# Kernel optimization log

Measured on AMD Instinct MI355X. Metric: run time of the kernel, lower is better.

## Reference

```python
import jax, jax.numpy as jnp
import numpy as np

N, M, D = 1024, 32, 512


def setup_inputs() -> dict:
    key = jax.random.key(0)
    k1, = jax.random.split(key, 1)
    emb = jax.random.normal(k1, (N, M, D), dtype=jnp.float32)
    emb = emb / jnp.linalg.norm(emb, axis=-1, keepdims=True)  # module expects normed embeddings
    return {
        "normed_embedding": emb,
        "n": N,
        "m": M,
        "ln_w": jnp.array(10.0, dtype=jnp.float32),
        "ln_b": jnp.array(-5.0, dtype=jnp.float32),
    }


def reference(normed_embedding, n, m, ln_w, ln_b):
    # normed_embedding: [N, M, D]
    ck = jnp.mean(normed_embedding, axis=1)          # [N, D] inclusive centroids
    sums = jnp.sum(normed_embedding, axis=1)         # [N, D]
    e = normed_embedding.reshape(n * m, -1)          # [NM, D]
    sims = jnp.matmul(e, ck.T)                       # [NM, N]

    # exclusive centroid for own speaker: cj = (sum_i - e_ij) / (m - 1)
    ex = jnp.sum(normed_embedding * (sums[:, None, :] - normed_embedding), axis=-1) / (m - 1)  # [N, M]
    rows = jnp.arange(n * m)
    spk = rows // m                                  # speaker label per row
    sims = sims.at[rows, spk].set(ex.reshape(-1))

    sims = jax.nn.sigmoid(ln_w * sims + ln_b)

    own = sims[rows, spk]                            # [NM]
    own_col = spk[:, None] == jnp.arange(n)[None, :]  # mask own speaker column
    max_other = jnp.max(jnp.where(own_col, -jnp.inf, sims), axis=-1)  # [NM]
    loss = jnp.mean(1.0 - own + max_other).reshape(1)

    preds = jnp.argmax(sims, axis=1)
    batch_acc = jnp.mean((preds == spk).astype(jnp.float32))
    return loss, batch_acc
```

## Files before the change

### kernel.cpp

```cpp
#include <hip/hip_runtime.h>


#define N_SPK 1024
#define M_UTT 32
#define D_DIM 512
#define NROWS (N_SPK * M_UTT)
#define NTILES 8
#define MTILES 256
#define NWG (MTILES * NTILES)
#define NKT 8

typedef __attribute__((ext_vector_type(4))) float f32x4;

__device__ __forceinline__ void gload_lds16(const void* g, void* l) {
    __builtin_amdgcn_global_load_lds(
        (const __attribute__((address_space(1))) unsigned int*)g,
        (__attribute__((address_space(3))) unsigned int*)l, 16, 0, 0);
}

__device__ __forceinline__ float sigmoidf(float x) {
    return 1.f / (1.f + __expf(-x));
}

__global__ void __launch_bounds__(256) prep_kernel(const float* __restrict__ emb,
                                                   const float* __restrict__ lnw,
                                                   unsigned int* __restrict__ e8,
                                                   unsigned int* __restrict__ ck8) {
    __shared__ float part[2][D_DIM];
    const int n = blockIdx.x;
    const int t = threadIdx.x;
    const int d4 = (t & 127) * 4;
    const int mh = t >> 7;
    const float* base = emb + (size_t)n * M_UTT * D_DIM;

    float4 acc = {0.f, 0.f, 0.f, 0.f};
#pragma unroll
    for (int mm = 0; mm < 16; ++mm) {
        const int m = mh * 16 + mm;
        const float4 v = *reinterpret_cast<const float4*>(base + m * D_DIM + d4);
        acc.x += v.x; acc.y += v.y; acc.z += v.z; acc.w += v.w;
        int w = __builtin_amdgcn_cvt_pk_fp8_f32(8.f * v.x, 8.f * v.y, 0, false);
        w = __builtin_amdgcn_cvt_pk_fp8_f32(8.f * v.z, 8.f * v.w, w, true);
        e8[(((size_t)(n * M_UTT + m)) * D_DIM + d4) >> 2] = (unsigned int)w;
    }
    *reinterpret_cast<float4*>(&part[mh][d4]) = acc;
    __syncthreads();
    if (t < 128) {
        const float sgn = (lnw[0] >= 0.f) ? 1.f : -1.f;
        const float sc = sgn * 0.5f;
        const int d = t * 4;
        const float4 a = *reinterpret_cast<const float4*>(&part[0][d]);
        const float4 b = *reinterpret_cast<const float4*>(&part[1][d]);
        int w = __builtin_amdgcn_cvt_pk_fp8_f32((a.x + b.x) * sc, (a.y + b.y) * sc, 0, false);
        w = __builtin_amdgcn_cvt_pk_fp8_f32((a.z + b.z) * sc, (a.w + b.w) * sc, w, true);
        ck8[(((size_t)n) * D_DIM + d) >> 2] = (unsigned int)w;
    }
}

__global__ void __launch_bounds__(256, 3)
gemm_kernel(const char* __restrict__ e8,
            const char* __restrict__ ck8,
            float* __restrict__ maxo_part,
            float* __restrict__ own_part) {
    __shared__ __align__(16) char buf[2][16384];
    __shared__ float redm[2][128];
    __shared__ float redo[2][128];

    const int tid  = threadIdx.x;
    const int lane = tid & 63;
    const int wv   = tid >> 6;
    const int lo   = lane & 15;
    const int hi   = lane >> 4;
    const int wm   = wv >> 1;
    const int wn   = wv & 1;

    const int raw   = blockIdx.x;
    const int xcd   = raw & 7;
    const int local = raw >> 3;
    const int mt    = xcd * 32 + (local >> 3);
    const int nt    = local & 7;
    const int r0    = mt * 128;
    const int n0    = nt * 128;

    const char* pA[2];
    const char* pB[2];
    int dA[2], dB[2];
#pragma unroll
    for (int j = 0; j < 2; ++j) {
        const int s   = j * 256 + tid;
        const int L   = s >> 3;
        const int l   = (s & 7) ^ (L & 7);
        const int row = 2 * L + (l >> 2);
        const int kch = l & 3;
        pA[j] = e8  + (size_t)(r0 + row) * D_DIM + kch * 16;
        pB[j] = ck8 + (size_t)(n0 + row) * D_DIM + kch * 16;
        dA[j] = s * 16;
        dB[j] = 8192 + s * 16;
    }

    auto stage = [&](int u) {
        char* bb = &buf[u & 1][0];
        const int ko = u * 64;
#pragma unroll
        for (int j = 0; j < 2; ++j) {
            gload_lds16(pA[j] + ko, bb + dA[j]);
            gload_lds16(pB[j] + ko, bb + dB[j]);
        }
    };

    stage(0);
    asm volatile("s_waitcnt vmcnt(0)" ::: "memory");
    __builtin_amdgcn_s_barrier();

    const int Lr    = lo >> 1;
    const int par   = lo & 1;
    const int phys0 = ((par << 2) | (hi >> 1))     ^ Lr;
    const int phys1 = ((par << 2) | 2 | (hi >> 1)) ^ Lr;
    const int a0 = (wm * 32 + Lr) * 128 + phys0 * 16 + (hi & 1) * 8;
    const int a1 = (wm * 32 + Lr) * 128 + phys1 * 16 + (hi & 1) * 8;
    const int b0 = 8192 + (wn * 32 + Lr) * 128 + phys0 * 16 + (hi & 1) * 8;
    const int b1 = 8192 + (wn * 32 + Lr) * 128 + phys1 * 16 + (hi & 1) * 8;

    f32x4 acc[4][4];
#pragma unroll
    for (int am = 0; am < 4; ++am)
#pragma unroll
        for (int an = 0; an < 4; ++an) acc[am][an] = (f32x4){0.f, 0.f, 0.f, 0.f};

    long a[4], b[4];

#pragma unroll
    for (int t = 0; t < NKT; ++t) {
        const char* bp = &buf[t & 1][0];
        if (t < NKT - 1) stage(t + 1);

#pragma unroll
        for (int am = 0; am < 4; ++am)
            a[am] = *reinterpret_cast<const long*>(bp + a0 + am * 1024);
#pragma unroll
        for (int an = 0; an < 4; ++an)
            b[an] = *reinterpret_cast<const long*>(bp + b0 + an * 1024);
        __builtin_amdgcn_s_setprio(1);
#pragma unroll
        for (int am = 0; am < 4; ++am)
#pragma unroll
            for (int an = 0; an < 4; ++an)
                acc[am][an] = __builtin_amdgcn_mfma_f32_16x16x32_fp8_fp8(
                    a[am], b[an], acc[am][an], 0, 0, 0);
        __builtin_amdgcn_s_setprio(0);

#pragma unroll
        for (int am = 0; am < 4; ++am)
            a[am] = *reinterpret_cast<const long*>(bp + a1 + am * 1024);
#pragma unroll
        for (int an = 0; an < 4; ++an)
            b[an] = *reinterpret_cast<const long*>(bp + b1 + an * 1024);
        __builtin_amdgcn_s_setprio(1);
#pragma unroll
        for (int am = 0; am < 4; ++am)
#pragma unroll
            for (int an = 0; an < 4; ++an)
                acc[am][an] = __builtin_amdgcn_mfma_f32_16x16x32_fp8_fp8(
                    a[am], b[an], acc[am][an], 0, 0, 0);
        __builtin_amdgcn_s_setprio(0);

        asm volatile("s_waitcnt lgkmcnt(0)" ::: "memory");
        if (t < NKT - 1) asm volatile("s_waitcnt vmcnt(0)" ::: "memory");
        __builtin_amdgcn_s_barrier();
    }

    const float NEG = -1e30f;
#pragma unroll
    for (int am = 0; am < 4; ++am) {
#pragma unroll
        for (int reg = 0; reg < 4; ++reg) {
            const int rl   = wm * 64 + am * 16 + hi * 4 + reg;
            const int rowg = r0 + rl;
            const int spk  = rowg >> 5;
            float m = NEG, o = NEG;
#pragma unroll
            for (int an = 0; an < 4; ++an) {
                const int col = n0 + wn * 64 + an * 16 + lo;
                const float v = acc[am][an][reg];
                const bool dg = (col == spk);
                o = dg ? v : o;
                m = fmaxf(m, dg ? NEG : v);
            }
#pragma unroll
            for (int mask = 1; mask < 16; mask <<= 1) {
                m = fmaxf(m, __shfl_xor(m, mask));
                o = fmaxf(o, __shfl_xor(o, mask));
            }
            if (lo == 0) {
                redm[wn][rl] = m;
                redo[wn][rl] = o;
            }
        }
    }
    __syncthreads();

    if (tid < 128) {
        const float mo = fmaxf(redm[0][tid], redm[1][tid]);
        maxo_part[(size_t)nt * NROWS + r0 + tid] = mo;
        if (nt == (mt >> 5)) {
            own_part[r0 + tid] = fmaxf(redo[0][tid], redo[1][tid]);
        }
    }
}

__global__ void __launch_bounds__(256) rowred_kernel(const float* __restrict__ maxo_part,
                                                     const float* __restrict__ own_part,
                                                     const float* __restrict__ lnw,
                                                     const float* __restrict__ lnb,
                                                     float* __restrict__ partsum) {
    const int r = blockIdx.x * 256 + threadIdx.x;
    const float lw = lnw[0], lb = lnb[0];
    const float sgn = (lw >= 0.f) ? 1.f : -1.f;
    const float alw = fabsf(lw);
    const float inv128 = 1.f / 128.f;

    float mo = maxo_part[r];
#pragma unroll
    for (int p = 1; p < NTILES; ++p)
        mo = fmaxf(mo, maxo_part[(size_t)p * NROWS + r]);
    const float O     = own_part[r];
    const float t_own = sgn * O * inv128;
    const float ex    = (32.f * t_own - 1.f) * (1.f / 31.f);
    const float own_s = sigmoidf(lw * ex + lb);
    const float mo_s  = sigmoidf(alw * mo * inv128 + lb);
    float loss = 1.f - own_s + mo_s;
    float corr = (sgn * ex >= mo * inv128) ? 1.f : 0.f;

#pragma unroll
    for (int mask = 1; mask < 64; mask <<= 1) {
        loss += __shfl_xor(loss, mask);
        corr += __shfl_xor(corr, mask);
    }
    __shared__ float sl[4], sc[4];
    const int wv = threadIdx.x >> 6;
    if ((threadIdx.x & 63) == 0) { sl[wv] = loss; sc[wv] = corr; }
    __syncthreads();
    if (threadIdx.x == 0) {
        partsum[blockIdx.x]       = sl[0] + sl[1] + sl[2] + sl[3];
        partsum[128 + blockIdx.x] = sc[0] + sc[1] + sc[2] + sc[3];
    }
}

__global__ void __launch_bounds__(128) final_kernel(const float* __restrict__ partsum,
                                                    float* __restrict__ out) {
    const int t = threadIdx.x;
    float l = partsum[t];
    float c = partsum[128 + t];
#pragma unroll
    for (int mask = 1; mask < 64; mask <<= 1) {
        l += __shfl_xor(l, mask);
        c += __shfl_xor(c, mask);
    }
    __shared__ float sl[2], sc[2];
    if ((t & 63) == 0) { sl[t >> 6] = l; sc[t >> 6] = c; }
    __syncthreads();
    if (t == 0) {
        out[0] = (sl[0] + sl[1]) * (1.f / (float)NROWS);
        out[1] = (sc[0] + sc[1]) * (1.f / (float)NROWS);
    }
}

extern "C" void kernel_launch(void* const* d_in, const int* in_sizes, int n_in,
                              void* d_out, int out_size, void* d_ws, size_t ws_size,
                              hipStream_t stream) {
    (void)in_sizes; (void)n_in; (void)out_size; (void)ws_size;
    const float* emb = (const float*)d_in[0];
    const float* lnw = (const float*)d_in[3];
    const float* lnb = (const float*)d_in[4];
    float* out = (float*)d_out;

    char* ws = (char*)d_ws;
    char* e8  = ws;
    char* ck8 = ws + (size_t)NROWS * D_DIM;
    float* maxo_part = (float*)(ck8 + (size_t)N_SPK * D_DIM);
    float* own_part  = (float*)((char*)maxo_part + (size_t)NTILES * NROWS * 4);
    float* partsum   = (float*)((char*)own_part + (size_t)NROWS * 4);

    prep_kernel<<<N_SPK, 256, 0, stream>>>(emb, lnw, (unsigned int*)e8, (unsigned int*)ck8);
    gemm_kernel<<<NWG, 256, 0, stream>>>(e8, ck8, maxo_part, own_part);
    rowred_kernel<<<NROWS / 256, 256, 0, stream>>>(maxo_part, own_part, lnw, lnb, partsum);
    final_kernel<<<1, 128, 0, stream>>>(partsum, out);
}
```

Before: 56.88 us.

## Triple-buffer GEMM LDS staging and permute fp8 layout for 16-byte fragment loads

The prep kernel now writes fp8 embeddings and centroids in a permuted K order, so that each lane's two MFMA k-slices sit next to each other. The GEMM can then fetch both with a single 16-byte LDS read instead of two 8-byte reads. The GEMM also moves from double to triple buffering: it prefetches two K-tiles ahead and waits with vmcnt(4) instead of draining all loads each iteration, to hide global-load latency. The cost is 48KB of LDS per workgroup instead of 32KB, which may lower occupancy under the 3-blocks-per-CU launch bound. The new layout must match exactly between the prep and GEMM kernels.

```diff
diff --git a/kernel.cpp b/kernel.cpp
--- a/kernel.cpp
+++ b/kernel.cpp
@@ -11,6 +11,7 @@
 #define NKT 8
 
 typedef __attribute__((ext_vector_type(4))) float f32x4;
+typedef __attribute__((ext_vector_type(2))) long long2v;
 
 __device__ __forceinline__ void gload_lds16(const void* g, void* l) {
     __builtin_amdgcn_global_load_lds(
@@ -24,36 +25,52 @@
 
 __global__ void __launch_bounds__(256) prep_kernel(const float* __restrict__ emb,
                                                    const float* __restrict__ lnw,
-                                                   unsigned int* __restrict__ e8,
-                                                   unsigned int* __restrict__ ck8) {
-    __shared__ float part[2][D_DIM];
+                                                   char* __restrict__ e8,
+                                                   char* __restrict__ ck8) {
+    __shared__ float part[4][D_DIM];
     const int n = blockIdx.x;
     const int t = threadIdx.x;
-    const int d4 = (t & 127) * 4;
-    const int mh = t >> 7;
-    const float* base = emb + (size_t)n * M_UTT * D_DIM;
-
-    float4 acc = {0.f, 0.f, 0.f, 0.f};
-#pragma unroll
-    for (int mm = 0; mm < 16; ++mm) {
-        const int m = mh * 16 + mm;
-        const float4 v = *reinterpret_cast<const float4*>(base + m * D_DIM + d4);
-        acc.x += v.x; acc.y += v.y; acc.z += v.z; acc.w += v.w;
-        int w = __builtin_amdgcn_cvt_pk_fp8_f32(8.f * v.x, 8.f * v.y, 0, false);
-        w = __builtin_amdgcn_cvt_pk_fp8_f32(8.f * v.z, 8.f * v.w, w, true);
-        e8[(((size_t)(n * M_UTT + m)) * D_DIM + d4) >> 2] = (unsigned int)w;
-    }
-    *reinterpret_cast<float4*>(&part[mh][d4]) = acc;
-    __syncthreads();
-    if (t < 128) {
-        const float sgn = (lnw[0] >= 0.f) ? 1.f : -1.f;
-        const float sc = sgn * 0.5f;
-        const int d = t * 4;
-        const float4 a = *reinterpret_cast<const float4*>(&part[0][d]);
-        const float4 b = *reinterpret_cast<const float4*>(&part[1][d]);
-        int w = __builtin_amdgcn_cvt_pk_fp8_f32((a.x + b.x) * sc, (a.y + b.y) * sc, 0, false);
-        w = __builtin_amdgcn_cvt_pk_fp8_f32((a.z + b.z) * sc, (a.w + b.w) * sc, w, true);
-        ck8[(((size_t)n) * D_DIM + d) >> 2] = (unsigned int)w;
+    const int q = t & 63;
+    const int g = t >> 6;
+    const int pdst = (q >> 3) * 64 + (q & 3) * 16 + ((q >> 2) & 1) * 8;
+    const float* base = emb + (size_t)n * M_UTT * D_DIM + q * 8;
+
+    float acc8[8];
+#pragma unroll
+    for (int j = 0; j < 8; ++j) acc8[j] = 0.f;
+
+#pragma unroll
+    for (int i = 0; i < 8; ++i) {
+        const int m = g * 8 + i;
+        const float4 v0 = *reinterpret_cast<const float4*>(base + m * D_DIM);
+        const float4 v1 = *reinterpret_cast<const float4*>(base + m * D_DIM + 4);
+        acc8[0] += v0.x; acc8[1] += v0.y; acc8[2] += v0.z; acc8[3] += v0.w;
+        acc8[4] += v1.x; acc8[5] += v1.y; acc8[6] += v1.z; acc8[7] += v1.w;
+        int w0 = __builtin_amdgcn_cvt_pk_fp8_f32(8.f * v0.x, 8.f * v0.y, 0, false);
+        w0 = __builtin_amdgcn_cvt_pk_fp8_f32(8.f * v0.z, 8.f * v0.w, w0, true);
+        int w1 = __builtin_amdgcn_cvt_pk_fp8_f32(8.f * v1.x, 8.f * v1.y, 0, false);
+        w1 = __builtin_amdgcn_cvt_pk_fp8_f32(8.f * v1.z, 8.f * v1.w, w1, true);
+        uint2 w; w.x = (unsigned)w0; w.y = (unsigned)w1;
+        *reinterpret_cast<uint2*>(e8 + (size_t)(n * M_UTT + m) * D_DIM + pdst) = w;
+    }
+#pragma unroll
+    for (int j = 0; j < 8; ++j) part[g][q * 8 + j] = acc8[j];
+    __syncthreads();
+
+    if (t < 64) {
+        const float sc = (lnw[0] >= 0.f) ? 0.5f : -0.5f;
+        float s[8];
+#pragma unroll
+        for (int j = 0; j < 8; ++j)
+            s[j] = (part[0][t * 8 + j] + part[1][t * 8 + j] +
+                    part[2][t * 8 + j] + part[3][t * 8 + j]) * sc;
+        int w0 = __builtin_amdgcn_cvt_pk_fp8_f32(s[0], s[1], 0, false);
+        w0 = __builtin_amdgcn_cvt_pk_fp8_f32(s[2], s[3], w0, true);
+        int w1 = __builtin_amdgcn_cvt_pk_fp8_f32(s[4], s[5], 0, false);
+        w1 = __builtin_amdgcn_cvt_pk_fp8_f32(s[6], s[7], w1, true);
+        uint2 w; w.x = (unsigned)w0; w.y = (unsigned)w1;
+        const int pd = (t >> 3) * 64 + (t & 3) * 16 + ((t >> 2) & 1) * 8;
+        *reinterpret_cast<uint2*>(ck8 + (size_t)n * D_DIM + pd) = w;
     }
 }
 
@@ -62,7 +79,7 @@
             const char* __restrict__ ck8,
             float* __restrict__ maxo_part,
             float* __restrict__ own_part) {
-    __shared__ __align__(16) char buf[2][16384];
+    __shared__ __align__(16) char buf[3][16384];
     __shared__ float redm[2][128];
     __shared__ float redo[2][128];
 
@@ -91,15 +108,15 @@
         const int L   = s >> 3;
         const int l   = (s & 7) ^ (L & 7);
         const int row = 2 * L + (l >> 2);
-        const int kch = l & 3;
-        pA[j] = e8  + (size_t)(r0 + row) * D_DIM + kch * 16;
-        pB[j] = ck8 + (size_t)(n0 + row) * D_DIM + kch * 16;
+        const int c   = l & 3;
+        pA[j] = e8  + (size_t)(r0 + row) * D_DIM + c * 16;
+        pB[j] = ck8 + (size_t)(n0 + row) * D_DIM + c * 16;
         dA[j] = s * 16;
         dB[j] = 8192 + s * 16;
     }
 
-    auto stage = [&](int u) {
-        char* bb = &buf[u & 1][0];
+    auto stage = [&](int u, int slot) {
+        char* bb = &buf[slot][0];
         const int ko = u * 64;
 #pragma unroll
         for (int j = 0; j < 2; ++j) {
@@ -108,18 +125,16 @@
         }
     };
 
-    stage(0);
-    asm volatile("s_waitcnt vmcnt(0)" ::: "memory");
+    stage(0, 0);
+    stage(1, 1);
+    asm volatile("s_waitcnt vmcnt(4)" ::: "memory");
     __builtin_amdgcn_s_barrier();
 
-    const int Lr    = lo >> 1;
+    const int swz   = (lo >> 1) & 7;
     const int par   = lo & 1;
-    const int phys0 = ((par << 2) | (hi >> 1))     ^ Lr;
-    const int phys1 = ((par << 2) | 2 | (hi >> 1)) ^ Lr;
-    const int a0 = (wm * 32 + Lr) * 128 + phys0 * 16 + (hi & 1) * 8;
-    const int a1 = (wm * 32 + Lr) * 128 + phys1 * 16 + (hi & 1) * 8;
-    const int b0 = 8192 + (wn * 32 + Lr) * 128 + phys0 * 16 + (hi & 1) * 8;
-    const int b1 = 8192 + (wn * 32 + Lr) * 128 + phys1 * 16 + (hi & 1) * 8;
+    const int physr = ((par << 2) | hi) ^ swz;
+    const int abase = (wm * 32 + (lo >> 1)) * 128 + physr * 16;
+    const int bbase = 8192 + (wn * 32 + (lo >> 1)) * 128 + physr * 16;
 
     f32x4 acc[4][4];
 #pragma unroll
@@ -127,45 +142,37 @@
 #pragma unroll
         for (int an = 0; an < 4; ++an) acc[am][an] = (f32x4){0.f, 0.f, 0.f, 0.f};
 
-    long a[4], b[4];
-
 #pragma unroll
     for (int t = 0; t < NKT; ++t) {
-        const char* bp = &buf[t & 1][0];
-        if (t < NKT - 1) stage(t + 1);
-
+        const char* bp = &buf[t % 3][0];
+        if (t + 2 < NKT) stage(t + 2, (t + 2) % 3);
+
+        long2v a2[4], b2[4];
 #pragma unroll
         for (int am = 0; am < 4; ++am)
-            a[am] = *reinterpret_cast<const long*>(bp + a0 + am * 1024);
+            a2[am] = *reinterpret_cast<const long2v*>(bp + abase + am * 1024);
 #pragma unroll
         for (int an = 0; an < 4; ++an)
-            b[an] = *reinterpret_cast<const long*>(bp + b0 + an * 1024);
+            b2[an] = *reinterpret_cast<const long2v*>(bp + bbase + an * 1024);
+
         __builtin_amdgcn_s_setprio(1);
 #pragma unroll
         for (int am = 0; am < 4; ++am)
 #pragma unroll
             for (int an = 0; an < 4; ++an)
                 acc[am][an] = __builtin_amdgcn_mfma_f32_16x16x32_fp8_fp8(
-                    a[am], b[an], acc[am][an], 0, 0, 0);
-        __builtin_amdgcn_s_setprio(0);
-
-#pragma unroll
-        for (int am = 0; am < 4; ++am)
-            a[am] = *reinterpret_cast<const long*>(bp + a1 + am * 1024);
-#pragma unroll
-        for (int an = 0; an < 4; ++an)
-            b[an] = *reinterpret_cast<const long*>(bp + b1 + an * 1024);
-        __builtin_amdgcn_s_setprio(1);
+                    a2[am][0], b2[an][0], acc[am][an], 0, 0, 0);
 #pragma unroll
         for (int am = 0; am < 4; ++am)
 #pragma unroll
             for (int an = 0; an < 4; ++an)
                 acc[am][an] = __builtin_amdgcn_mfma_f32_16x16x32_fp8_fp8(
-                    a[am], b[an], acc[am][an], 0, 0, 0);
+                    a2[am][1], b2[an][1], acc[am][an], 0, 0, 0);
         __builtin_amdgcn_s_setprio(0);
 
         asm volatile("s_waitcnt lgkmcnt(0)" ::: "memory");
-        if (t < NKT - 1) asm volatile("s_waitcnt vmcnt(0)" ::: "memory");
+        if (t < NKT - 2)       asm volatile("s_waitcnt vmcnt(4)" ::: "memory");
+        else if (t == NKT - 2) asm volatile("s_waitcnt vmcnt(0)" ::: "memory");
         __builtin_amdgcn_s_barrier();
     }
 
@@ -281,7 +288,7 @@
     float* own_part  = (float*)((char*)maxo_part + (size_t)NTILES * NROWS * 4);
     float* partsum   = (float*)((char*)own_part + (size_t)NROWS * 4);
 
-    prep_kernel<<<N_SPK, 256, 0, stream>>>(emb, lnw, (unsigned int*)e8, (unsigned int*)ck8);
+    prep_kernel<<<N_SPK, 256, 0, stream>>>(emb, lnw, e8, ck8);
     gemm_kernel<<<NWG, 256, 0, stream>>>(e8, ck8, maxo_part, own_part);
     rowred_kernel<<<NROWS / 256, 256, 0, stream>>>(maxo_part, own_part, lnw, lnb, partsum);
     final_kernel<<<1, 128, 0, stream>>>(partsum, out);
```

After: 64.71 us. +13.8%, slower.

## Switch GEMM to 32x32x64 scaled FP8 MFMA with triple-buffered LDS pipeline

Applied to the files above, without the earlier changes.

Replaces the 16x16x32 FP8 MFMAs with the gfx950 scaled 32x32x64 f8f6f4 MFMA using unit scales, so each wave issues 4 large MFMAs per K-tile instead of 32 small ones and reads 16-byte LDS fragments. LDS staging goes from double to triple buffering, prefetching two tiles ahead with partial vmcnt waits. The epilogue row/column mapping and the shuffle reduction width are adapted to the 32x32 output layout. This drops the occupancy hint of 3 and raises LDS use, which may reduce occupancy.

```diff
diff --git a/kernel.cpp b/kernel.cpp
--- a/kernel.cpp
+++ b/kernel.cpp
@@ -10,7 +10,9 @@
 #define NWG (MTILES * NTILES)
 #define NKT 8
 
-typedef __attribute__((ext_vector_type(4))) float f32x4;
+typedef __attribute__((ext_vector_type(16))) float f32x16;
+typedef __attribute__((ext_vector_type(8)))  int   i32x8;
+typedef __attribute__((ext_vector_type(4)))  int   i32x4;
 
 __device__ __forceinline__ void gload_lds16(const void* g, void* l) {
     __builtin_amdgcn_global_load_lds(
@@ -57,20 +59,20 @@
     }
 }
 
-__global__ void __launch_bounds__(256, 3)
+__global__ void __launch_bounds__(256)
 gemm_kernel(const char* __restrict__ e8,
             const char* __restrict__ ck8,
             float* __restrict__ maxo_part,
             float* __restrict__ own_part) {
-    __shared__ __align__(16) char buf[2][16384];
+    __shared__ __align__(16) char buf[3][16384];
     __shared__ float redm[2][128];
     __shared__ float redo[2][128];
 
     const int tid  = threadIdx.x;
     const int lane = tid & 63;
     const int wv   = tid >> 6;
-    const int lo   = lane & 15;
-    const int hi   = lane >> 4;
+    const int l31  = lane & 31;
+    const int kg   = lane >> 5;
     const int wm   = wv >> 1;
     const int wn   = wv & 1;
 
@@ -91,15 +93,15 @@
         const int L   = s >> 3;
         const int l   = (s & 7) ^ (L & 7);
         const int row = 2 * L + (l >> 2);
-        const int kch = l & 3;
-        pA[j] = e8  + (size_t)(r0 + row) * D_DIM + kch * 16;
-        pB[j] = ck8 + (size_t)(n0 + row) * D_DIM + kch * 16;
+        const int c   = l & 3;
+        pA[j] = e8  + (size_t)(r0 + row) * D_DIM + c * 16;
+        pB[j] = ck8 + (size_t)(n0 + row) * D_DIM + c * 16;
         dA[j] = s * 16;
         dB[j] = 8192 + s * 16;
     }
 
-    auto stage = [&](int u) {
-        char* bb = &buf[u & 1][0];
+    auto stage = [&](int u, int slot) {
+        char* bb = &buf[slot][0];
         const int ko = u * 64;
 #pragma unroll
         for (int j = 0; j < 2; ++j) {
@@ -108,90 +110,97 @@
         }
     };
 
-    stage(0);
-    asm volatile("s_waitcnt vmcnt(0)" ::: "memory");
+    stage(0, 0);
+    stage(1, 1);
+    asm volatile("s_waitcnt vmcnt(4)" ::: "memory");
     __builtin_amdgcn_s_barrier();
 
-    const int Lr    = lo >> 1;
-    const int par   = lo & 1;
-    const int phys0 = ((par << 2) | (hi >> 1))     ^ Lr;
-    const int phys1 = ((par << 2) | 2 | (hi >> 1)) ^ Lr;
-    const int a0 = (wm * 32 + Lr) * 128 + phys0 * 16 + (hi & 1) * 8;
-    const int a1 = (wm * 32 + Lr) * 128 + phys1 * 16 + (hi & 1) * 8;
-    const int b0 = 8192 + (wn * 32 + Lr) * 128 + phys0 * 16 + (hi & 1) * 8;
-    const int b1 = 8192 + (wn * 32 + Lr) * 128 + phys1 * 16 + (hi & 1) * 8;
-
-    f32x4 acc[4][4];
-#pragma unroll
-    for (int am = 0; am < 4; ++am)
-#pragma unroll
-        for (int an = 0; an < 4; ++an) acc[am][an] = (f32x4){0.f, 0.f, 0.f, 0.f};
-
-    long a[4], b[4];
+    int aoff[2][2], boff[2][2];
+#pragma unroll
+    for (int am = 0; am < 2; ++am) {
+        const int r = wm * 64 + am * 32 + l31;
+        const int L = r >> 1, u = r & 1, s = L & 7;
+#pragma unroll
+        for (int h = 0; h < 2; ++h)
+            aoff[am][h] = L * 128 + ((((u << 2) | (kg * 2 + h)) ^ s) * 16);
+    }
+#pragma unroll
+    for (int an = 0; an < 2; ++an) {
+        const int r = wn * 64 + an * 32 + l31;
+        const int L = r >> 1, u = r & 1, s = L & 7;
+#pragma unroll
+        for (int h = 0; h < 2; ++h)
+            boff[an][h] = 8192 + L * 128 + ((((u << 2) | (kg * 2 + h)) ^ s) * 16);
+    }
+
+    f32x16 acc00 = {0.f}, acc01 = {0.f}, acc10 = {0.f}, acc11 = {0.f};
+#pragma unroll
+    for (int i = 0; i < 16; ++i) { acc00[i] = 0.f; acc01[i] = 0.f; acc10[i] = 0.f; acc11[i] = 0.f; }
+
+    const int SCALE1 = 0x7F7F7F7F;
 
 #pragma unroll
     for (int t = 0; t < NKT; ++t) {
-        const char* bp = &buf[t & 1][0];
-        if (t < NKT - 1) stage(t + 1);
-
-#pragma unroll
-        for (int am = 0; am < 4; ++am)
-            a[am] = *reinterpret_cast<const long*>(bp + a0 + am * 1024);
-#pragma unroll
-        for (int an = 0; an < 4; ++an)
-            b[an] = *reinterpret_cast<const long*>(bp + b0 + an * 1024);
+        const char* bp = &buf[t % 3][0];
+        if (t + 2 < NKT) stage(t + 2, (t + 2) % 3);
+
+        const i32x4 a0l = *reinterpret_cast<const i32x4*>(bp + aoff[0][0]);
+        const i32x4 a0h = *reinterpret_cast<const i32x4*>(bp + aoff[0][1]);
+        const i32x4 a1l = *reinterpret_cast<const i32x4*>(bp + aoff[1][0]);
+        const i32x4 a1h = *reinterpret_cast<const i32x4*>(bp + aoff[1][1]);
+        const i32x4 b0l = *reinterpret_cast<const i32x4*>(bp + boff[0][0]);
+        const i32x4 b0h = *reinterpret_cast<const i32x4*>(bp + boff[0][1]);
+        const i32x4 b1l = *reinterpret_cast<const i32x4*>(bp + boff[1][0]);
+        const i32x4 b1h = *reinterpret_cast<const i32x4*>(bp + boff[1][1]);
+
+        const i32x8 A0 = __builtin_shufflevector(a0l, a0h, 0, 1, 2, 3, 4, 5, 6, 7);
+        const i32x8 A1 = __builtin_shufflevector(a1l, a1h, 0, 1, 2, 3, 4, 5, 6, 7);
+        const i32x8 B0 = __builtin_shufflevector(b0l, b0h, 0, 1, 2, 3, 4, 5, 6, 7);
+        const i32x8 B1 = __builtin_shufflevector(b1l, b1h, 0, 1, 2, 3, 4, 5, 6, 7);
+
         __builtin_amdgcn_s_setprio(1);
-#pragma unroll
-        for (int am = 0; am < 4; ++am)
-#pragma unroll
-            for (int an = 0; an < 4; ++an)
-                acc[am][an] = __builtin_amdgcn_mfma_f32_16x16x32_fp8_fp8(
-                    a[am], b[an], acc[am][an], 0, 0, 0);
+        acc00 = __builtin_amdgcn_mfma_scale_f32_32x32x64_f8f6f4(
+            A0, B0, acc00, 0, 0, 0, SCALE1, 0, SCALE1);
+        acc01 = __builtin_amdgcn_mfma_scale_f32_32x32x64_f8f6f4(
+            A0, B1, acc01, 0, 0, 0, SCALE1, 0, SCALE1);
+        acc10 = __builtin_amdgcn_mfma_scale_f32_32x32x64_f8f6f4(
+            A1, B0, acc10, 0, 0, 0, SCALE1, 0, SCALE1);
+        acc11 = __builtin_amdgcn_mfma_scale_f32_32x32x64_f8f6f4(
+            A1, B1, acc11, 0, 0, 0, SCALE1, 0, SCALE1);
         __builtin_amdgcn_s_setprio(0);
 
-#pragma unroll
-        for (int am = 0; am < 4; ++am)
-            a[am] = *reinterpret_cast<const long*>(bp + a1 + am * 1024);
-#pragma unroll
-        for (int an = 0; an < 4; ++an)
-            b[an] = *reinterpret_cast<const long*>(bp + b1 + an * 1024);
-        __builtin_amdgcn_s_setprio(1);
-#pragma unroll
-        for (int am = 0; am < 4; ++am)
-#pragma unroll
-            for (int an = 0; an < 4; ++an)
-                acc[am][an] = __builtin_amdgcn_mfma_f32_16x16x32_fp8_fp8(
-                    a[am], b[an], acc[am][an], 0, 0, 0);
-        __builtin_amdgcn_s_setprio(0);
-
         asm volatile("s_waitcnt lgkmcnt(0)" ::: "memory");
-        if (t < NKT - 1) asm volatile("s_waitcnt vmcnt(0)" ::: "memory");
+        if (t < NKT - 2)       asm volatile("s_waitcnt vmcnt(4)" ::: "memory");
+        else if (t == NKT - 2) asm volatile("s_waitcnt vmcnt(0)" ::: "memory");
         __builtin_amdgcn_s_barrier();
     }
 
     const float NEG = -1e30f;
 #pragma unroll
-    for (int am = 0; am < 4; ++am) {
-#pragma unroll
-        for (int reg = 0; reg < 4; ++reg) {
-            const int rl   = wm * 64 + am * 16 + hi * 4 + reg;
-            const int rowg = r0 + rl;
-            const int spk  = rowg >> 5;
+    for (int am = 0; am < 2; ++am) {
+#pragma unroll
+        for (int reg = 0; reg < 16; ++reg) {
+            const int rl  = wm * 64 + am * 32 + (reg & 3) + 8 * (reg >> 2) + 4 * kg;
+            const int spk = (r0 + rl) >> 5;
             float m = NEG, o = NEG;
-#pragma unroll
-            for (int an = 0; an < 4; ++an) {
-                const int col = n0 + wn * 64 + an * 16 + lo;
-                const float v = acc[am][an][reg];
-                const bool dg = (col == spk);
-                o = dg ? v : o;
-                m = fmaxf(m, dg ? NEG : v);
+            {
+                const int col0 = n0 + wn * 64 + l31;
+                const float v0 = am ? acc10[reg] : acc00[reg];
+                const bool dg0 = (col0 == spk);
+                o = dg0 ? v0 : o;
+                m = fmaxf(m, dg0 ? NEG : v0);
+                const int col1 = col0 + 32;
+                const float v1 = am ? acc11[reg] : acc01[reg];
+                const bool dg1 = (col1 == spk);
+                o = dg1 ? v1 : o;
+                m = fmaxf(m, dg1 ? NEG : v1);
             }
 #pragma unroll
-            for (int mask = 1; mask < 16; mask <<= 1) {
+            for (int mask = 1; mask < 32; mask <<= 1) {
                 m = fmaxf(m, __shfl_xor(m, mask));
                 o = fmaxf(o, __shfl_xor(o, mask));
             }
-            if (lo == 0) {
+            if (l31 == 0) {
                 redm[wn][rl] = m;
                 redo[wn][rl] = o;
             }
```

Result: slower. 112.5 us (+97.8%).

## Triple-buffer LDS stages and permute fp8 layout for 128-bit fragment loads

Applied to the files above, without the earlier changes.

The prep kernel now writes fp8 embeddings and centroids in a permuted K order, so that each lane's two MFMA k-slices sit next to each other in memory. The GEMM can then fetch both with a single 16-byte LDS read instead of two 8-byte reads. The GEMM also moves from double to triple buffering, prefetching two k-tiles ahead and waiting with vmcnt(4), so global-to-LDS loads overlap more with MFMA work. The cost is more LDS per block, which may reduce occupancy under the launch bound of 3 blocks, plus more complex wait-count logic.

```diff
diff --git a/kernel.cpp b/kernel.cpp
--- a/kernel.cpp
+++ b/kernel.cpp
@@ -11,6 +11,7 @@
 #define NKT 8
 
 typedef __attribute__((ext_vector_type(4))) float f32x4;
+typedef __attribute__((ext_vector_type(2))) long long2v;
 
 __device__ __forceinline__ void gload_lds16(const void* g, void* l) {
     __builtin_amdgcn_global_load_lds(
@@ -31,6 +32,7 @@
     const int t = threadIdx.x;
     const int d4 = (t & 127) * 4;
     const int mh = t >> 7;
+    const int od = (d4 & ~63) + ((d4 >> 3) & 3) * 16 + ((d4 >> 5) & 1) * 8 + (d4 & 4);
     const float* base = emb + (size_t)n * M_UTT * D_DIM;
 
     float4 acc = {0.f, 0.f, 0.f, 0.f};
@@ -41,7 +43,7 @@
         acc.x += v.x; acc.y += v.y; acc.z += v.z; acc.w += v.w;
         int w = __builtin_amdgcn_cvt_pk_fp8_f32(8.f * v.x, 8.f * v.y, 0, false);
         w = __builtin_amdgcn_cvt_pk_fp8_f32(8.f * v.z, 8.f * v.w, w, true);
-        e8[(((size_t)(n * M_UTT + m)) * D_DIM + d4) >> 2] = (unsigned int)w;
+        e8[(((size_t)(n * M_UTT + m)) * D_DIM + od) >> 2] = (unsigned int)w;
     }
     *reinterpret_cast<float4*>(&part[mh][d4]) = acc;
     __syncthreads();
@@ -49,11 +51,12 @@
         const float sgn = (lnw[0] >= 0.f) ? 1.f : -1.f;
         const float sc = sgn * 0.5f;
         const int d = t * 4;
+        const int odc = (d & ~63) + ((d >> 3) & 3) * 16 + ((d >> 5) & 1) * 8 + (d & 4);
         const float4 a = *reinterpret_cast<const float4*>(&part[0][d]);
         const float4 b = *reinterpret_cast<const float4*>(&part[1][d]);
         int w = __builtin_amdgcn_cvt_pk_fp8_f32((a.x + b.x) * sc, (a.y + b.y) * sc, 0, false);
         w = __builtin_amdgcn_cvt_pk_fp8_f32((a.z + b.z) * sc, (a.w + b.w) * sc, w, true);
-        ck8[(((size_t)n) * D_DIM + d) >> 2] = (unsigned int)w;
+        ck8[(((size_t)n) * D_DIM + odc) >> 2] = (unsigned int)w;
     }
 }
 
@@ -62,7 +65,7 @@
             const char* __restrict__ ck8,
             float* __restrict__ maxo_part,
             float* __restrict__ own_part) {
-    __shared__ __align__(16) char buf[2][16384];
+    __shared__ __align__(16) char buf[3][16384];
     __shared__ float redm[2][128];
     __shared__ float redo[2][128];
 
@@ -91,15 +94,15 @@
         const int L   = s >> 3;
         const int l   = (s & 7) ^ (L & 7);
         const int row = 2 * L + (l >> 2);
-        const int kch = l & 3;
-        pA[j] = e8  + (size_t)(r0 + row) * D_DIM + kch * 16;
-        pB[j] = ck8 + (size_t)(n0 + row) * D_DIM + kch * 16;
+        const int c   = l & 3;
+        pA[j] = e8  + (size_t)(r0 + row) * D_DIM + c * 16;
+        pB[j] = ck8 + (size_t)(n0 + row) * D_DIM + c * 16;
         dA[j] = s * 16;
         dB[j] = 8192 + s * 16;
     }
 
-    auto stage = [&](int u) {
-        char* bb = &buf[u & 1][0];
+    auto stage = [&](int u, int slot) {
+        char* bb = &buf[slot][0];
         const int ko = u * 64;
 #pragma unroll
         for (int j = 0; j < 2; ++j) {
@@ -108,18 +111,16 @@
         }
     };
 
-    stage(0);
-    asm volatile("s_waitcnt vmcnt(0)" ::: "memory");
+    stage(0, 0);
+    stage(1, 1);
+    asm volatile("s_waitcnt vmcnt(4)" ::: "memory");
     __builtin_amdgcn_s_barrier();
 
-    const int Lr    = lo >> 1;
+    const int swz   = (lo >> 1) & 7;
     const int par   = lo & 1;
-    const int phys0 = ((par << 2) | (hi >> 1))     ^ Lr;
-    const int phys1 = ((par << 2) | 2 | (hi >> 1)) ^ Lr;
-    const int a0 = (wm * 32 + Lr) * 128 + phys0 * 16 + (hi & 1) * 8;
-    const int a1 = (wm * 32 + Lr) * 128 + phys1 * 16 + (hi & 1) * 8;
-    const int b0 = 8192 + (wn * 32 + Lr) * 128 + phys0 * 16 + (hi & 1) * 8;
-    const int b1 = 8192 + (wn * 32 + Lr) * 128 + phys1 * 16 + (hi & 1) * 8;
+    const int physr = ((par << 2) | hi) ^ swz;
+    const int abase = (wm * 32 + (lo >> 1)) * 128 + physr * 16;
+    const int bbase = 8192 + (wn * 32 + (lo >> 1)) * 128 + physr * 16;
 
     f32x4 acc[4][4];
 #pragma unroll
@@ -127,45 +128,37 @@
 #pragma unroll
         for (int an = 0; an < 4; ++an) acc[am][an] = (f32x4){0.f, 0.f, 0.f, 0.f};
 
-    long a[4], b[4];
-
 #pragma unroll
     for (int t = 0; t < NKT; ++t) {
-        const char* bp = &buf[t & 1][0];
-        if (t < NKT - 1) stage(t + 1);
-
+        const char* bp = &buf[t % 3][0];
+        if (t + 2 < NKT) stage(t + 2, (t + 2) % 3);
+
+        long2v a2[4], b2[4];
 #pragma unroll
         for (int am = 0; am < 4; ++am)
-            a[am] = *reinterpret_cast<const long*>(bp + a0 + am * 1024);
+            a2[am] = *reinterpret_cast<const long2v*>(bp + abase + am * 1024);
 #pragma unroll
         for (int an = 0; an < 4; ++an)
-            b[an] = *reinterpret_cast<const long*>(bp + b0 + an * 1024);
+            b2[an] = *reinterpret_cast<const long2v*>(bp + bbase + an * 1024);
+
         __builtin_amdgcn_s_setprio(1);
 #pragma unroll
         for (int am = 0; am < 4; ++am)
 #pragma unroll
             for (int an = 0; an < 4; ++an)
                 acc[am][an] = __builtin_amdgcn_mfma_f32_16x16x32_fp8_fp8(
-                    a[am], b[an], acc[am][an], 0, 0, 0);
-        __builtin_amdgcn_s_setprio(0);
-
-#pragma unroll
-        for (int am = 0; am < 4; ++am)
-            a[am] = *reinterpret_cast<const long*>(bp + a1 + am * 1024);
-#pragma unroll
-        for (int an = 0; an < 4; ++an)
-            b[an] = *reinterpret_cast<const long*>(bp + b1 + an * 1024);
-        __builtin_amdgcn_s_setprio(1);
+                    a2[am][0], b2[an][0], acc[am][an], 0, 0, 0);
 #pragma unroll
         for (int am = 0; am < 4; ++am)
 #pragma unroll
             for (int an = 0; an < 4; ++an)
                 acc[am][an] = __builtin_amdgcn_mfma_f32_16x16x32_fp8_fp8(
-                    a[am], b[an], acc[am][an], 0, 0, 0);
+                    a2[am][1], b2[an][1], acc[am][an], 0, 0, 0);
         __builtin_amdgcn_s_setprio(0);
 
         asm volatile("s_waitcnt lgkmcnt(0)" ::: "memory");
-        if (t < NKT - 1) asm volatile("s_waitcnt vmcnt(0)" ::: "memory");
+        if (t < NKT - 2)       asm volatile("s_waitcnt vmcnt(4)" ::: "memory");
+        else if (t == NKT - 2) asm volatile("s_waitcnt vmcnt(0)" ::: "memory");
         __builtin_amdgcn_s_barrier();
     }
 
```

Measured after the change: 55.29 us. 2.8% less time.
